# Performance work log

Measured on AMD Instinct MI355X. Metric: run time of the kernel, lower is better.

## Reference

```python
import jax, jax.numpy as jnp
import numpy as np

N = 100000      # nodes
E = 1600000     # edges (avg degree 16)
F_IN = 32       # node_features
F_OUT = 32      # filters
K = 2           # Chebyshev order


def setup_inputs() -> dict:
    key = jax.random.key(0)
    ks = jax.random.split(key, 8)
    x = jax.random.normal(ks[0], (N, F_IN), dtype=jnp.float32)
    edge_index = jax.random.randint(ks[1], (2, E), 0, N, dtype=jnp.int32).astype(jnp.int64)
    edge_weight = jax.random.uniform(ks[2], (E,), dtype=jnp.float32)
    s_in = 1.0 / np.sqrt(F_IN)
    s_out = 1.0 / np.sqrt(F_OUT)
    # gate order: i, f, c, o
    Wx = jax.random.normal(ks[3], (4, K, F_IN, F_OUT), dtype=jnp.float32) * s_in
    bx = jnp.zeros((4, F_OUT), dtype=jnp.float32)
    Wh = jax.random.normal(ks[4], (4, K, F_OUT, F_OUT), dtype=jnp.float32) * s_out
    bh = jnp.zeros((4, F_OUT), dtype=jnp.float32)
    wc = jax.random.normal(ks[5], (3, F_OUT), dtype=jnp.float32) * 0.1  # peephole i, f, o
    b_gate = jnp.zeros((4, F_OUT), dtype=jnp.float32)
    lin_w = jax.random.normal(ks[6], (F_OUT, 1), dtype=jnp.float32) * s_out
    lin_b = jnp.zeros((1,), dtype=jnp.float32)
    return dict(x=x, edge_index=edge_index, edge_weight=edge_weight, Wx=Wx, bx=bx,
                Wh=Wh, bh=bh, wc=wc, b_gate=b_gate, lin_w=lin_w, lin_b=lin_b)


def _cheb_norm(src, dst, w, num_nodes):
    # ChebConv 'sym' normalization with lambda_max = 2.0:
    # scaled Laplacian L_hat = L_sym - I has zero diagonal; off-diagonal entries are
    # -D^{-1/2} A D^{-1/2}. Self loops removed (equivalently: weight zeroed).
    w = jnp.where(src == dst, 0.0, w)
    deg = jax.ops.segment_sum(w, src, num_segments=num_nodes)
    dinv = jnp.where(deg > 0, jax.lax.rsqrt(jnp.where(deg > 0, deg, 1.0)), 0.0)
    return -dinv[src] * w * dinv[dst]


def _forward(x, src, dst, norm, Wx, bx, Wh, bh, wc, b_gate, lin_w, lin_b):
    n = x.shape[0]

    def cheb(inp, W, b):
        # K=2 Chebyshev conv: Tx_0 = inp, Tx_1 = L_hat @ inp (sparse gather/scatter)
        tx1 = jax.ops.segment_sum(norm[:, None] * inp[src], dst, num_segments=n)
        return inp @ W[0] + tx1 @ W[1] + b

    H = jnp.zeros((n, Wh.shape[-1]), dtype=x.dtype)
    C = jnp.zeros_like(H)
    I = jax.nn.sigmoid(cheb(x, Wx[0], bx[0]) + cheb(H, Wh[0], bh[0]) + wc[0] * C + b_gate[0])
    Fg = jax.nn.sigmoid(cheb(x, Wx[1], bx[1]) + cheb(H, Wh[1], bh[1]) + wc[1] * C + b_gate[1])
    T = jnp.tanh(cheb(x, Wx[2], bx[2]) + cheb(H, Wh[2], bh[2]) + b_gate[2])
    C = Fg * C + I * T
    O = jax.nn.sigmoid(cheb(x, Wx[3], bx[3]) + cheb(H, Wh[3], bh[3]) + wc[2] * C + b_gate[3])
    H = O * jnp.tanh(C)
    return jax.nn.relu(H) @ lin_w + lin_b  # [N, 1]


def reference(x, edge_index, edge_weight, Wx, bx, Wh, bh, wc, b_gate, lin_w, lin_b):
    src, dst = edge_index[0], edge_index[1]
    norm = _cheb_norm(src, dst, edge_weight, x.shape[0])
    return _forward(x, src, dst, norm, Wx, bx, Wh, bh, wc, b_gate, lin_w, lin_b)
```

## Files before the change

### kernel.cpp

```cpp
#include <hip/hip_runtime.h>


#define FDIM 32
#define MAX_N 100000
#define MAX_E 1600000
#define CBSH 8
#define CB 256
#define MAX_NB ((MAX_N + CB - 1) / CB)
#define NBLK 512
#define SCAN_TILE 2048
#define GNB 64
#define PERBLK 3136

typedef int   iv4 __attribute__((ext_vector_type(4)));
typedef float fv4 __attribute__((ext_vector_type(4)));
__device__ __forceinline__ iv4 nt_i4(const int* p)   { return __builtin_nontemporal_load((const iv4*)p); }
__device__ __forceinline__ fv4 nt_f4(const float* p) { return __builtin_nontemporal_load((const fv4*)p); }

__device__ float g_deg[MAX_N];
__device__ int   g_part2[2 * MAX_NB * NBLK + 1];
__device__ int   g_blk[1024];
__device__ uint2 g_rec[MAX_E];
__device__ uint2 g_srec[MAX_E];
__device__ int   g_row[MAX_N + 1];
__device__ __attribute__((aligned(16))) int   g_src2[MAX_E];
__device__ __attribute__((aligned(16))) float g_nrm2[MAX_E];
__device__ float g_tx1[MAX_N * FDIM];

__device__ __forceinline__ int scanned(int idx) {
    return g_part2[idx] + g_blk[idx >> 11];
}

__global__ __launch_bounds__(256) void hist2_kernel(const int* __restrict__ ei,
                                                    int E, int n_nodes, int nbuck,
                                                    int per_blk) {
    __shared__ int hd[MAX_NB];
    __shared__ int hs[MAX_NB];
    for (int i = threadIdx.x; i < nbuck; i += 256) { hd[i] = 0; hs[i] = 0; }
    __syncthreads();
    int start = blockIdx.x * per_blk;
    int end = start + per_blk;
    if (end > E) end = E;
    for (int base = start; base < end; base += 1024) {
        int e = base + threadIdx.x * 4;
        if (e + 4 <= end) {
            int4 s4 = *(const int4*)(ei + e);
            int4 d4 = *(const int4*)(ei + E + e);
#define H2(S, D) if ((unsigned)(S) < (unsigned)n_nodes && (unsigned)(D) < (unsigned)n_nodes) { \
                atomicAdd(&hd[(D) >> CBSH], 1); atomicAdd(&hs[(S) >> CBSH], 1); }
            H2(s4.x, d4.x) H2(s4.y, d4.y) H2(s4.z, d4.z) H2(s4.w, d4.w)
#undef H2
        } else if (e < end) {
            for (int q = e; q < end; ++q) {
                int s = ei[q], d = ei[E + q];
                if ((unsigned)s >= (unsigned)n_nodes || (unsigned)d >= (unsigned)n_nodes)
                    continue;
                atomicAdd(&hd[d >> CBSH], 1);
                atomicAdd(&hs[s >> CBSH], 1);
            }
        }
    }
    __syncthreads();
    for (int i = threadIdx.x; i < nbuck; i += 256) {
        g_part2[i * NBLK + blockIdx.x] = hd[i];
        g_part2[(nbuck + i) * NBLK + blockIdx.x] = hs[i];
    }
    if (blockIdx.x == 0 && threadIdx.x == 0)
        g_part2[2 * nbuck * NBLK] = 0;
}

__global__ __launch_bounds__(256) void scan1_kernel(int n) {
    __shared__ int sh[256];
    int tid = threadIdx.x;
    int base = blockIdx.x * SCAN_TILE + tid * 8;
    int v[8];
#pragma unroll
    for (int i = 0; i < 8; ++i) v[i] = (base + i < n) ? g_part2[base + i] : 0;
    int tsum = 0;
#pragma unroll
    for (int i = 0; i < 8; ++i) tsum += v[i];
    sh[tid] = tsum;
    __syncthreads();
    for (int off = 1; off < 256; off <<= 1) {
        int t = (tid >= off) ? sh[tid - off] : 0;
        __syncthreads();
        sh[tid] += t;
        __syncthreads();
    }
    if (tid == 255) g_blk[blockIdx.x] = sh[255];
    int run = sh[tid] - tsum;
#pragma unroll
    for (int i = 0; i < 8; ++i) {
        if (base + i < n) g_part2[base + i] = run;
        run += v[i];
    }
}

__global__ __launch_bounds__(256) void scan2_kernel(int nb) {
    __shared__ int sh[256];
    int tid = threadIdx.x;
    int base = tid * 4;
    int v[4];
#pragma unroll
    for (int i = 0; i < 4; ++i) v[i] = (base + i < nb) ? g_blk[base + i] : 0;
    int tsum = v[0] + v[1] + v[2] + v[3];
    sh[tid] = tsum;
    __syncthreads();
    for (int off = 1; off < 256; off <<= 1) {
        int t = (tid >= off) ? sh[tid - off] : 0;
        __syncthreads();
        sh[tid] += t;
        __syncthreads();
    }
    int run = sh[tid] - tsum;
#pragma unroll
    for (int i = 0; i < 4; ++i) {
        if (base + i < nb) g_blk[base + i] = run;
        run += v[i];
    }
}

__global__ __launch_bounds__(256) void scatter_burst_kernel(const int* __restrict__ ei,
                                                            const float* __restrict__ w,
                                                            int E, int n_nodes, int nbuck,
                                                            int per_blk) {
    __shared__ int   cnt[512];
    __shared__ int   sc[512];
    __shared__ int   gb[MAX_NB];
    __shared__ int   cur[MAX_NB];
    __shared__ uint2 staged[PERBLK];
    __shared__ int   gpos[PERBLK];
    int tid = threadIdx.x;
    int blk = blockIdx.x;
    int start = blk * per_blk;
    int end = start + per_blk;
    if (end > E) end = E;

    for (int phase = 0; phase < 2; ++phase) {
        cnt[tid] = 0; cnt[tid + 256] = 0;
        __syncthreads();
        for (int i = tid; i < nbuck; i += 256) {
            int flat = (phase * nbuck + i) * NBLK + blk;
            int g0 = scanned(flat);
            int g1 = scanned(flat + 1);
            gb[i] = g0 - phase * E;
            cnt[i] = g1 - g0;
        }
        __syncthreads();
        sc[tid] = cnt[tid]; sc[tid + 256] = cnt[tid + 256];
        __syncthreads();
        for (int off = 1; off < 512; off <<= 1) {
            int v0 = (tid >= off) ? sc[tid - off] : 0;
            int v1 = sc[tid + 256 - off];
            __syncthreads();
            sc[tid] += v0; sc[tid + 256] += v1;
            __syncthreads();
        }
        for (int i = tid; i < nbuck; i += 256) cur[i] = sc[i] - cnt[i];
        __syncthreads();
#define SB1(S, D, W)                                                            \
        {   int s = (S), d = (D);                                               \
            if ((unsigned)s < (unsigned)n_nodes && (unsigned)d < (unsigned)n_nodes) { \
                int key = phase ? s : d;                                        \
                int bin = key >> CBSH;                                          \
                float w0 = (s == d) ? 0.f : (W);           \
                unsigned pay = phase ? (unsigned)(s & (CB - 1))                 \
                    : (((unsigned)s << CBSH) | (unsigned)(d & (CB - 1)));       \
                int p = atomicAdd(&cur[bin], 1);                \
                staged[p] = make_uint2(pay, __float_as_uint(w0));               \
                gpos[p] = gb[bin] + (p - (sc[bin] - cnt[bin]));                 \
            } }
        for (int base = start; base < end; base += 1024) {
            int e = base + tid * 4;
            if (e + 4 <= end) {
                iv4 s4 = nt_i4(ei + e);
                iv4 d4 = nt_i4(ei + E + e);
                fv4 w4 = nt_f4(w + e);
                SB1(s4[0], d4[0], w4[0]) SB1(s4[1], d4[1], w4[1])
                SB1(s4[2], d4[2], w4[2]) SB1(s4[3], d4[3], w4[3])
            } else if (e < end) {
                for (int q = e; q < end; ++q) SB1(ei[q], ei[E + q], w[q])
            }
        }
#undef SB1
        __syncthreads();
        int tot = sc[511];
        if (phase == 0) {
            for (int t = tid; t < tot; t += 256) g_rec[gpos[t]] = staged[t];
        } else {
            for (int t = tid; t < tot; t += 256) g_srec[gpos[t]] = staged[t];
        }
        __syncthreads();
    }
}

__global__ __launch_bounds__(1024) void deg_sum_kernel(int E, int n_nodes, int nbuck) {
    __shared__ float ldeg[CB];
    int b = blockIdx.x;
    int rs = scanned((nbuck + b) * NBLK) - E;
    int re = scanned((nbuck + b + 1) * NBLK) - E;
    if (threadIdx.x < CB) ldeg[threadIdx.x] = 0.f;
    __syncthreads();
    for (int i = rs + threadIdx.x; i < re; i += 1024) {
        uint2 r = g_srec[i];
        atomicAdd(&ldeg[r.x], __uint_as_float(r.y));
    }
    __syncthreads();
    if (threadIdx.x < CB) {
        int node = (b << CBSH) + threadIdx.x;
        if (node < n_nodes) {
            float dg = ldeg[threadIdx.x];
            g_deg[node] = (dg > 0.f) ? rsqrtf(dg) : 0.f;
        }
    }
}

__global__ __launch_bounds__(1024) void fine_sort_kernel(int E, int n_nodes, int nbuck) {
    __shared__ int cnt[CB];
    __shared__ int cur[CB];
    __shared__ float dv[CB];
    __shared__ int wsum[4];
    int b = blockIdx.x;
    int rs = scanned(b * NBLK);
    int re = scanned((b + 1) * NBLK);
    if (threadIdx.x < CB) {
        int tid = threadIdx.x;
        cnt[tid] = 0;
        int node = (b << CBSH) + tid;
        dv[tid] = (node < n_nodes) ? g_deg[node] : 0.f;
    }
    __syncthreads();
    for (int i = rs + threadIdx.x; i < re; i += 1024)
        atomicAdd(&cnt[g_rec[i].x & (CB - 1)], 1);
    __syncthreads();
    if (threadIdx.x < CB) {
        int tid = threadIdx.x;
        int lane = tid & 63;
        int wave = tid >> 6;
        int v = cnt[tid];
        int inc = v;
#pragma unroll
        for (int off = 1; off < 64; off <<= 1) {
            int t = __shfl_up(inc, off, 64);
            if (lane >= off) inc += t;
        }
        if (lane == 63) wsum[wave] = inc;
        __syncthreads();
        int wo = 0;
#pragma unroll
        for (int ww = 0; ww < 4; ++ww) wo += (ww < wave) ? wsum[ww] : 0;
        int start = rs + wo + (inc - v);
        cur[tid] = start;
        int node = (b << CBSH) + tid;
        if (node < n_nodes) g_row[node] = start;
    } else {
        __syncthreads();
    }
    if (b == nbuck - 1 && threadIdx.x == 0) g_row[n_nodes] = re;
    __syncthreads();
    for (int i = rs + threadIdx.x; i < re; i += 1024) {
        uint2 r = g_rec[i];
        int s = (int)(r.x >> CBSH);
        int loc = r.x & (CB - 1);
        float nrm = -g_deg[s] * __uint_as_float(r.y) * dv[loc];
        int pos = atomicAdd(&cur[loc], 1);
        g_src2[pos] = s;
        g_nrm2[pos] = nrm;
    }
}

__global__ __launch_bounds__(256) void gather_kernel(const float* __restrict__ x,
                                                     int n_nodes) {
    int t = blockIdx.x * blockDim.x + threadIdx.x;
    int node = t >> 5;
    int f = t & 31;
    if (node >= n_nodes) return;
    int i = g_row[node];
    int end = g_row[node + 1];
    float acc = 0.f, accB = 0.f;
    while (i < end && (i & 3)) {
        acc += g_nrm2[i] * x[g_src2[i] * FDIM + f];
        ++i;
    }
    for (; i + 8 <= end; i += 8) {
        iv4 sa = nt_i4(g_src2 + i);
        iv4 sb = nt_i4(g_src2 + i + 4);
        fv4 na = nt_f4(g_nrm2 + i);
        fv4 nb = nt_f4(g_nrm2 + i + 4);
        float xa0 = x[sa[0] * FDIM + f], xa1 = x[sa[1] * FDIM + f];
        float xa2 = x[sa[2] * FDIM + f], xa3 = x[sa[3] * FDIM + f];
        float xb0 = x[sb[0] * FDIM + f], xb1 = x[sb[1] * FDIM + f];
        float xb2 = x[sb[2] * FDIM + f], xb3 = x[sb[3] * FDIM + f];
        acc  += na[0] * xa0 + na[1] * xa1 + na[2] * xa2 + na[3] * xa3;
        accB += nb[0] * xb0 + nb[1] * xb1 + nb[2] * xb2 + nb[3] * xb3;
    }
    for (; i + 4 <= end; i += 4) {
        iv4 s4 = nt_i4(g_src2 + i);
        fv4 n4 = nt_f4(g_nrm2 + i);
        acc += n4[0] * x[s4[0] * FDIM + f] + n4[1] * x[s4[1] * FDIM + f]
             + n4[2] * x[s4[2] * FDIM + f] + n4[3] * x[s4[3] * FDIM + f];
    }
    for (; i < end; ++i) acc += g_nrm2[i] * x[g_src2[i] * FDIM + f];
    g_tx1[node * FDIM + f] = acc + accB;
}

__global__ __launch_bounds__(256, 4) void gates64_kernel(
    const float* __restrict__ x,
    const float* __restrict__ Wx, const float* __restrict__ bx,
    const float* __restrict__ bh, const float* __restrict__ wc,
    const float* __restrict__ bg, const float* __restrict__ lin_w,
    const float* __restrict__ lin_b, float* __restrict__ out, int n_nodes) {
    __shared__ float Ws[3 * 2048];
    __shared__ float xs[GNB * FDIM];
    __shared__ float ts[GNB * FDIM];

    for (int idx = threadIdx.x; idx < 512; idx += 256) {
        *(float4*)&Ws[idx * 4]        = *(const float4*)&Wx[0 * 2048 + idx * 4];
        *(float4*)&Ws[2048 + idx * 4] = *(const float4*)&Wx[2 * 2048 + idx * 4];
        *(float4*)&Ws[4096 + idx * 4] = *(const float4*)&Wx[3 * 2048 + idx * 4];
    }
    int node0 = blockIdx.x * GNB;
    for (int t = threadIdx.x; t < GNB * FDIM / 4; t += 256) {
        int q = t * 4;
        int n = node0 + (q >> 5);
        float4 xv = make_float4(0.f, 0.f, 0.f, 0.f);
        float4 tv = make_float4(0.f, 0.f, 0.f, 0.f);
        if (n < n_nodes) {
            xv = *(const float4*)&x[n * FDIM + (q & 31)];
            tv = *(const float4*)&g_tx1[n * FDIM + (q & 31)];
        }
        *(float4*)&xs[q] = xv;
        *(float4*)&ts[q] = tv;
    }
    __syncthreads();

    int j   = threadIdx.x & 31;
    int grp = threadIdx.x >> 5;

    float ai0=0.f,ai1=0.f,ai2=0.f,ai3=0.f,ai4=0.f,ai5=0.f,ai6=0.f,ai7=0.f;
    float ac0=0.f,ac1=0.f,ac2=0.f,ac3=0.f,ac4=0.f,ac5=0.f,ac6=0.f,ac7=0.f;
    float ao0=0.f,ao1=0.f,ao2=0.f,ao3=0.f,ao4=0.f,ao5=0.f,ao6=0.f,ao7=0.f;
    const float* xr = &xs[(grp * 8) * FDIM];
    const float* tr = &ts[(grp * 8) * FDIM];
    for (int k4 = 0; k4 < 32; k4 += 4) {
        float4 xv0 = *(const float4*)(xr + 0 * FDIM + k4);
        float4 xv1 = *(const float4*)(xr + 1 * FDIM + k4);
        float4 xv2 = *(const float4*)(xr + 2 * FDIM + k4);
        float4 xv3 = *(const float4*)(xr + 3 * FDIM + k4);
        float4 xv4 = *(const float4*)(xr + 4 * FDIM + k4);
        float4 xv5 = *(const float4*)(xr + 5 * FDIM + k4);
        float4 xv6 = *(const float4*)(xr + 6 * FDIM + k4);
        float4 xv7 = *(const float4*)(xr + 7 * FDIM + k4);
        float4 tv0 = *(const float4*)(tr + 0 * FDIM + k4);
        float4 tv1 = *(const float4*)(tr + 1 * FDIM + k4);
        float4 tv2 = *(const float4*)(tr + 2 * FDIM + k4);
        float4 tv3 = *(const float4*)(tr + 3 * FDIM + k4);
        float4 tv4 = *(const float4*)(tr + 4 * FDIM + k4);
        float4 tv5 = *(const float4*)(tr + 5 * FDIM + k4);
        float4 tv6 = *(const float4*)(tr + 6 * FDIM + k4);
        float4 tv7 = *(const float4*)(tr + 7 * FDIM + k4);
#define KSTEP(kc, COMP)                                        \
        {   int o0 = (k4 + kc) * 32 + j;                       \
            float wi0 = Ws[o0],        wi1 = Ws[1024 + o0];    \
            float wg0 = Ws[2048 + o0], wg1 = Ws[3072 + o0];    \
            float wo0 = Ws[4096 + o0], wo1 = Ws[5120 + o0];    \
            ai0 += xv0.COMP * wi0 + tv0.COMP * wi1;            \
            ac0 += xv0.COMP * wg0 + tv0.COMP * wg1;            \
            ao0 += xv0.COMP * wo0 + tv0.COMP * wo1;            \
            ai1 += xv1.COMP * wi0 + tv1.COMP * wi1;            \
            ac1 += xv1.COMP * wg0 + tv1.COMP * wg1;            \
            ao1 += xv1.COMP * wo0 + tv1.COMP * wo1;            \
            ai2 += xv2.COMP * wi0 + tv2.COMP * wi1;            \
            ac2 += xv2.COMP * wg0 + tv2.COMP * wg1;            \
            ao2 += xv2.COMP * wo0 + tv2.COMP * wo1;            \
            ai3 += xv3.COMP * wi0 + tv3.COMP * wi1;            \
            ac3 += xv3.COMP * wg0 + tv3.COMP * wg1;            \
            ao3 += xv3.COMP * wo0 + tv3.COMP * wo1;            \
            ai4 += xv4.COMP * wi0 + tv4.COMP * wi1;            \
            ac4 += xv4.COMP * wg0 + tv4.COMP * wg1;            \
            ao4 += xv4.COMP * wo0 + tv4.COMP * wo1;            \
            ai5 += xv5.COMP * wi0 + tv5.COMP * wi1;            \
            ac5 += xv5.COMP * wg0 + tv5.COMP * wg1;            \
            ao5 += xv5.COMP * wo0 + tv5.COMP * wo1;            \
            ai6 += xv6.COMP * wi0 + tv6.COMP * wi1;            \
            ac6 += xv6.COMP * wg0 + tv6.COMP * wg1;            \
            ao6 += xv6.COMP * wo0 + tv6.COMP * wo1;            \
            ai7 += xv7.COMP * wi0 + tv7.COMP * wi1;            \
            ac7 += xv7.COMP * wg0 + tv7.COMP * wg1;            \
            ao7 += xv7.COMP * wo0 + tv7.COMP * wo1;            \
        }
        KSTEP(0, x) KSTEP(1, y) KSTEP(2, z) KSTEP(3, w)
#undef KSTEP
    }

    float bi = bx[0 * 32 + j] + bh[0 * 32 + j] + bg[0 * 32 + j];
    float bc = bx[2 * 32 + j] + bh[2 * 32 + j] + bg[2 * 32 + j];
    float bo = bx[3 * 32 + j] + bh[3 * 32 + j] + bg[3 * 32 + j];
    float wcp = wc[2 * 32 + j];
    float lwj = lin_w[j];
    float lb0 = lin_b[0];

#define GOUT(m, AI, AC, AO)                                            \
    {   int n = node0 + grp * 8 + m;                                   \
        float I = 1.f / (1.f + __expf(-(AI + bi)));                    \
        float T = tanhf(AC + bc);                                      \
        float C = I * T;                                               \
        float O = 1.f / (1.f + __expf(-(AO + bo + wcp * C)));          \
        float H = O * tanhf(C);                                        \
        float r = fmaxf(H, 0.f) * lwj;                                 \
        _Pragma("unroll")                                              \
        for (int mm = 16; mm > 0; mm >>= 1) r += __shfl_xor(r, mm, 32);\
        if (j == 0 && n < n_nodes) out[n] = r + lb0; }
    GOUT(0, ai0, ac0, ao0) GOUT(1, ai1, ac1, ao1)
    GOUT(2, ai2, ac2, ao2) GOUT(3, ai3, ac3, ao3)
    GOUT(4, ai4, ac4, ao4) GOUT(5, ai5, ac5, ao5)
    GOUT(6, ai6, ac6, ao6) GOUT(7, ai7, ac7, ao7)
#undef GOUT
}

extern "C" void kernel_launch(void* const* d_in, const int* in_sizes, int n_in,
                              void* d_out, int out_size, void* d_ws, size_t ws_size,
                              hipStream_t stream) {
    const float* x     = (const float*)d_in[0];
    const int*   ei    = (const int*)d_in[1];
    const float* w     = (const float*)d_in[2];
    const float* Wx    = (const float*)d_in[3];
    const float* bx    = (const float*)d_in[4];
    const float* bh    = (const float*)d_in[6];
    const float* wc    = (const float*)d_in[7];
    const float* bg    = (const float*)d_in[8];
    const float* lin_w = (const float*)d_in[9];
    const float* lin_b = (const float*)d_in[10];
    float*       out   = (float*)d_out;

    int n_nodes = in_sizes[0] / FDIM;
    if (n_nodes > MAX_N) n_nodes = MAX_N;
    int E = in_sizes[2];
    if (E > MAX_E) E = MAX_E;

    int nbuck   = (n_nodes + CB - 1) >> CBSH;
    int per_blk = (((E + NBLK - 1) / NBLK) + 3) & ~3;
    int n_scan  = 2 * nbuck * NBLK + 1;
    int nb_scan = (n_scan + SCAN_TILE - 1) / SCAN_TILE;

    hist2_kernel<<<NBLK, 256, 0, stream>>>(ei, E, n_nodes, nbuck, per_blk);
    scan1_kernel<<<nb_scan, 256, 0, stream>>>(n_scan);
    scan2_kernel<<<1, 256, 0, stream>>>(nb_scan);
    scatter_burst_kernel<<<NBLK, 256, 0, stream>>>(ei, w, E, n_nodes, nbuck, per_blk);
    deg_sum_kernel<<<nbuck, 1024, 0, stream>>>(E, n_nodes, nbuck);
    fine_sort_kernel<<<nbuck, 1024, 0, stream>>>(E, n_nodes, nbuck);
    {
        long long tot = (long long)n_nodes * 32;
        gather_kernel<<<(int)((tot + 255) / 256), 256, 0, stream>>>(x, n_nodes);
    }
    gates64_kernel<<<(n_nodes + GNB - 1) / GNB, 256, 0, stream>>>(
        x, Wx, bx, bh, wc, bg, lin_w, lin_b, out, n_nodes);
}
```

Measured before the change: 248.1 us.

## Fold block-offset scan into consumers and fuse degree with fine sort

Drops the single-block second-level scan kernel. Each consumer block now recomputes the scan of the tile totals in shared memory. The degree-sum and fine-sort kernels are merged into one kernel that also writes a source-side degree-prescaled copy of x. The destination-side degree factor is applied once per node in the gather, which removes the per-edge random g_deg lookup in the sort. This cuts two launches and one dependency, at the cost of redundant small scans per block and an extra N×32 buffer write and read.

```diff
diff --git a/kernel.cpp b/kernel.cpp
--- a/kernel.cpp
+++ b/kernel.cpp
@@ -25,11 +25,8 @@
 __device__ int   g_row[MAX_N + 1];
 __device__ __attribute__((aligned(16))) int   g_src2[MAX_E];
 __device__ __attribute__((aligned(16))) float g_nrm2[MAX_E];
+__device__ __attribute__((aligned(16))) float g_xs2[MAX_N * FDIM];
 __device__ float g_tx1[MAX_N * FDIM];
-
-__device__ __forceinline__ int scanned(int idx) {
-    return g_part2[idx] + g_blk[idx >> 11];
-}
 
 __global__ __launch_bounds__(256) void hist2_kernel(const int* __restrict__ ei,
                                                     int E, int n_nodes, int nbuck,
@@ -96,34 +93,11 @@
     }
 }
 
-__global__ __launch_bounds__(256) void scan2_kernel(int nb) {
-    __shared__ int sh[256];
-    int tid = threadIdx.x;
-    int base = tid * 4;
-    int v[4];
-#pragma unroll
-    for (int i = 0; i < 4; ++i) v[i] = (base + i < nb) ? g_blk[base + i] : 0;
-    int tsum = v[0] + v[1] + v[2] + v[3];
-    sh[tid] = tsum;
-    __syncthreads();
-    for (int off = 1; off < 256; off <<= 1) {
-        int t = (tid >= off) ? sh[tid - off] : 0;
-        __syncthreads();
-        sh[tid] += t;
-        __syncthreads();
-    }
-    int run = sh[tid] - tsum;
-#pragma unroll
-    for (int i = 0; i < 4; ++i) {
-        if (base + i < nb) g_blk[base + i] = run;
-        run += v[i];
-    }
-}
-
 __global__ __launch_bounds__(256) void scatter_burst_kernel(const int* __restrict__ ei,
                                                             const float* __restrict__ w,
                                                             int E, int n_nodes, int nbuck,
-                                                            int per_blk) {
+                                                            int per_blk, int ntile) {
+    __shared__ int   toff[256];
     __shared__ int   cnt[512];
     __shared__ int   sc[512];
     __shared__ int   gb[MAX_NB];
@@ -136,13 +110,26 @@
     int end = start + per_blk;
     if (end > E) end = E;
 
+    int orig = (tid < ntile) ? g_blk[tid] : 0;
+    toff[tid] = orig;
+    __syncthreads();
+    for (int off = 1; off < 256; off <<= 1) {
+        int v = (tid >= off) ? toff[tid - off] : 0;
+        __syncthreads();
+        toff[tid] += v;
+        __syncthreads();
+    }
+    toff[tid] -= orig;
+    __syncthreads();
+#define SCN(idx) (g_part2[idx] + toff[(idx) >> 11])
+
     for (int phase = 0; phase < 2; ++phase) {
         cnt[tid] = 0; cnt[tid + 256] = 0;
         __syncthreads();
         for (int i = tid; i < nbuck; i += 256) {
             int flat = (phase * nbuck + i) * NBLK + blk;
-            int g0 = scanned(flat);
-            int g1 = scanned(flat + 1);
+            int g0 = SCN(flat);
+            int g1 = SCN(flat + 1);
             gb[i] = g0 - phase * E;
             cnt[i] = g1 - g0;
         }
@@ -192,85 +179,101 @@
         }
         __syncthreads();
     }
-}
-
-__global__ __launch_bounds__(1024) void deg_sum_kernel(int E, int n_nodes, int nbuck) {
+#undef SCN
+}
+
+__global__ __launch_bounds__(1024) void sortdeg_kernel(const float* __restrict__ x,
+                                                       int E, int n_nodes, int nbuck,
+                                                       int ntile) {
+    __shared__ int   toff[256];
+    __shared__ int   cnt[CB];
+    __shared__ int   cur[CB];
     __shared__ float ldeg[CB];
+    __shared__ int   wsum[4];
+    int tid = threadIdx.x;
     int b = blockIdx.x;
-    int rs = scanned((nbuck + b) * NBLK) - E;
-    int re = scanned((nbuck + b + 1) * NBLK) - E;
-    if (threadIdx.x < CB) ldeg[threadIdx.x] = 0.f;
-    __syncthreads();
-    for (int i = rs + threadIdx.x; i < re; i += 1024) {
+
+    int orig = 0;
+    if (tid < 256) { orig = (tid < ntile) ? g_blk[tid] : 0; toff[tid] = orig; }
+    __syncthreads();
+    for (int off = 1; off < 256; off <<= 1) {
+        int v = (tid < 256 && tid >= off) ? toff[tid - off] : 0;
+        __syncthreads();
+        if (tid < 256) toff[tid] += v;
+        __syncthreads();
+    }
+    if (tid < 256) toff[tid] -= orig;
+    if (tid < CB) { cnt[tid] = 0; ldeg[tid] = 0.f; }
+    __syncthreads();
+#define SCN(idx) (g_part2[idx] + toff[(idx) >> 11])
+    int rsD = SCN(b * NBLK);
+    int reD = SCN((b + 1) * NBLK);
+    int rsS = SCN((nbuck + b) * NBLK) - E;
+    int reS = SCN((nbuck + b + 1) * NBLK) - E;
+#undef SCN
+
+    for (int i = rsD + tid; i < reD; i += 1024)
+        atomicAdd(&cnt[g_rec[i].x & (CB - 1)], 1);
+    for (int i = rsS + tid; i < reS; i += 1024) {
         uint2 r = g_srec[i];
         atomicAdd(&ldeg[r.x], __uint_as_float(r.y));
     }
     __syncthreads();
-    if (threadIdx.x < CB) {
-        int node = (b << CBSH) + threadIdx.x;
+
+    if (tid < CB) {
+        float dg = ldeg[tid];
+        float dv = (dg > 0.f) ? rsqrtf(dg) : 0.f;
+        ldeg[tid] = dv;
+        int node = (b << CBSH) + tid;
+        if (node < n_nodes) g_deg[node] = dv;
+    }
+    __syncthreads();
+    for (int t = tid; t < CB * FDIM / 4; t += 1024) {
+        int q = t * 4;
+        int loc = q >> 5;
+        int node = (b << CBSH) + loc;
         if (node < n_nodes) {
-            float dg = ldeg[threadIdx.x];
-            g_deg[node] = (dg > 0.f) ? rsqrtf(dg) : 0.f;
-        }
-    }
-}
-
-__global__ __launch_bounds__(1024) void fine_sort_kernel(int E, int n_nodes, int nbuck) {
-    __shared__ int cnt[CB];
-    __shared__ int cur[CB];
-    __shared__ float dv[CB];
-    __shared__ int wsum[4];
-    int b = blockIdx.x;
-    int rs = scanned(b * NBLK);
-    int re = scanned((b + 1) * NBLK);
-    if (threadIdx.x < CB) {
-        int tid = threadIdx.x;
-        cnt[tid] = 0;
-        int node = (b << CBSH) + tid;
-        dv[tid] = (node < n_nodes) ? g_deg[node] : 0.f;
-    }
-    __syncthreads();
-    for (int i = rs + threadIdx.x; i < re; i += 1024)
-        atomicAdd(&cnt[g_rec[i].x & (CB - 1)], 1);
-    __syncthreads();
-    if (threadIdx.x < CB) {
-        int tid = threadIdx.x;
+            fv4 xv = *(const fv4*)&x[node * FDIM + (q & 31)];
+            float dv = ldeg[loc];
+            xv[0] *= dv; xv[1] *= dv; xv[2] *= dv; xv[3] *= dv;
+            *(fv4*)&g_xs2[node * FDIM + (q & 31)] = xv;
+        }
+    }
+
+    {
         int lane = tid & 63;
         int wave = tid >> 6;
-        int v = cnt[tid];
+        int v = (tid < CB) ? cnt[tid] : 0;
         int inc = v;
 #pragma unroll
         for (int off = 1; off < 64; off <<= 1) {
             int t = __shfl_up(inc, off, 64);
             if (lane >= off) inc += t;
         }
-        if (lane == 63) wsum[wave] = inc;
-        __syncthreads();
-        int wo = 0;
+        if (tid < CB && lane == 63) wsum[wave] = inc;
+        __syncthreads();
+        if (tid < CB) {
+            int wo = 0;
 #pragma unroll
-        for (int ww = 0; ww < 4; ++ww) wo += (ww < wave) ? wsum[ww] : 0;
-        int start = rs + wo + (inc - v);
-        cur[tid] = start;
-        int node = (b << CBSH) + tid;
-        if (node < n_nodes) g_row[node] = start;
-    } else {
-        __syncthreads();
-    }
-    if (b == nbuck - 1 && threadIdx.x == 0) g_row[n_nodes] = re;
-    __syncthreads();
-    for (int i = rs + threadIdx.x; i < re; i += 1024) {
+            for (int ww = 0; ww < 4; ++ww) wo += (ww < wave) ? wsum[ww] : 0;
+            int start = rsD + wo + (inc - v);
+            cur[tid] = start;
+            int node = (b << CBSH) + tid;
+            if (node < n_nodes) g_row[node] = start;
+        }
+    }
+    if (b == nbuck - 1 && tid == 0) g_row[n_nodes] = reD;
+    __syncthreads();
+    for (int i = rsD + tid; i < reD; i += 1024) {
         uint2 r = g_rec[i];
-        int s = (int)(r.x >> CBSH);
         int loc = r.x & (CB - 1);
-        float nrm = -g_deg[s] * __uint_as_float(r.y) * dv[loc];
         int pos = atomicAdd(&cur[loc], 1);
-        g_src2[pos] = s;
-        g_nrm2[pos] = nrm;
-    }
-}
-
-__global__ __launch_bounds__(256) void gather_kernel(const float* __restrict__ x,
-                                                     int n_nodes) {
+        g_src2[pos] = (int)(r.x >> CBSH);
+        g_nrm2[pos] = -__uint_as_float(r.y);
+    }
+}
+
+__global__ __launch_bounds__(256) void gather_kernel(int n_nodes) {
     int t = blockIdx.x * blockDim.x + threadIdx.x;
     int node = t >> 5;
     int f = t & 31;
@@ -279,7 +282,7 @@
     int end = g_row[node + 1];
     float acc = 0.f, accB = 0.f;
     while (i < end && (i & 3)) {
-        acc += g_nrm2[i] * x[g_src2[i] * FDIM + f];
+        acc += g_nrm2[i] * g_xs2[g_src2[i] * FDIM + f];
         ++i;
     }
     for (; i + 8 <= end; i += 8) {
@@ -287,21 +290,22 @@
         iv4 sb = nt_i4(g_src2 + i + 4);
         fv4 na = nt_f4(g_nrm2 + i);
         fv4 nb = nt_f4(g_nrm2 + i + 4);
-        float xa0 = x[sa[0] * FDIM + f], xa1 = x[sa[1] * FDIM + f];
-        float xa2 = x[sa[2] * FDIM + f], xa3 = x[sa[3] * FDIM + f];
-        float xb0 = x[sb[0] * FDIM + f], xb1 = x[sb[1] * FDIM + f];
-        float xb2 = x[sb[2] * FDIM + f], xb3 = x[sb[3] * FDIM + f];
+        float xa0 = g_xs2[sa[0] * FDIM + f], xa1 = g_xs2[sa[1] * FDIM + f];
+        float xa2 = g_xs2[sa[2] * FDIM + f], xa3 = g_xs2[sa[3] * FDIM + f];
+        float xb0 = g_xs2[sb[0] * FDIM + f], xb1 = g_xs2[sb[1] * FDIM + f];
+        float xb2 = g_xs2[sb[2] * FDIM + f], xb3 = g_xs2[sb[3] * FDIM + f];
         acc  += na[0] * xa0 + na[1] * xa1 + na[2] * xa2 + na[3] * xa3;
         accB += nb[0] * xb0 + nb[1] * xb1 + nb[2] * xb2 + nb[3] * xb3;
     }
     for (; i + 4 <= end; i += 4) {
         iv4 s4 = nt_i4(g_src2 + i);
         fv4 n4 = nt_f4(g_nrm2 + i);
-        acc += n4[0] * x[s4[0] * FDIM + f] + n4[1] * x[s4[1] * FDIM + f]
-             + n4[2] * x[s4[2] * FDIM + f] + n4[3] * x[s4[3] * FDIM + f];
-    }
-    for (; i < end; ++i) acc += g_nrm2[i] * x[g_src2[i] * FDIM + f];
-    g_tx1[node * FDIM + f] = acc + accB;
+        acc += n4[0] * g_xs2[s4[0] * FDIM + f] + n4[1] * g_xs2[s4[1] * FDIM + f]
+             + n4[2] * g_xs2[s4[2] * FDIM + f] + n4[3] * g_xs2[s4[3] * FDIM + f];
+    }
+    for (; i < end; ++i) acc += g_nrm2[i] * g_xs2[g_src2[i] * FDIM + f];
+    float dvn = g_deg[node];
+    g_tx1[node * FDIM + f] = dvn * (acc + accB);
 }
 
 __global__ __launch_bounds__(256, 4) void gates64_kernel(
@@ -445,13 +449,12 @@
 
     hist2_kernel<<<NBLK, 256, 0, stream>>>(ei, E, n_nodes, nbuck, per_blk);
     scan1_kernel<<<nb_scan, 256, 0, stream>>>(n_scan);
-    scan2_kernel<<<1, 256, 0, stream>>>(nb_scan);
-    scatter_burst_kernel<<<NBLK, 256, 0, stream>>>(ei, w, E, n_nodes, nbuck, per_blk);
-    deg_sum_kernel<<<nbuck, 1024, 0, stream>>>(E, n_nodes, nbuck);
-    fine_sort_kernel<<<nbuck, 1024, 0, stream>>>(E, n_nodes, nbuck);
+    scatter_burst_kernel<<<NBLK, 256, 0, stream>>>(ei, w, E, n_nodes, nbuck,
+                                                   per_blk, nb_scan);
+    sortdeg_kernel<<<nbuck, 1024, 0, stream>>>(x, E, n_nodes, nbuck, nb_scan);
     {
         long long tot = (long long)n_nodes * 32;
-        gather_kernel<<<(int)((tot + 255) / 256), 256, 0, stream>>>(x, n_nodes);
+        gather_kernel<<<(int)((tot + 255) / 256), 256, 0, stream>>>(n_nodes);
     }
     gates64_kernel<<<(n_nodes + GNB - 1) / GNB, 256, 0, stream>>>(
         x, Wx, bx, bh, wc, bg, lin_w, lin_b, out, n_nodes);
```

New measurement: 254.7 us. +2.7%, slower.
